# Kernel optimization log

Hardware: AMD Instinct MI355X
Metric: run time of the kernel (lower is better)

Reference implementation:

```python
import jax, jax.numpy as jnp
import numpy as np

THRESH = 0.7  # similarity_threshold from __init__
EPS = 1e-8    # torch cosine_similarity eps


def setup_inputs() -> dict:
    key = jax.random.key(0)
    ks = jax.random.split(key, 7)
    B, D, F, H, M, NMEM = 65536, 512, 10, 512, 256, 1024
    return {
        "query_features": jax.random.normal(ks[0], (B, D), jnp.float32),
        "B_mat": jax.random.normal(ks[1], (D, F), jnp.float32),
        "W1": jax.random.normal(ks[2], (2 * F, H), jnp.float32) * 0.05,
        "b1": jax.random.normal(ks[3], (H,), jnp.float32) * 0.01,
        "W2": jax.random.normal(ks[4], (H, M), jnp.float32) * 0.05,
        "b2": jax.random.normal(ks[5], (M,), jnp.float32) * 0.01,
        "memory_bank": jax.random.normal(ks[6], (NMEM, M), jnp.float32),
    }


def reference(query_features, B_mat, W1, b1, W2, b2, memory_bank):
    # Fourier features (eq. 8): [B, 2F]
    xp = query_features @ B_mat
    ff = jnp.concatenate([jnp.sin(xp), jnp.cos(xp)], axis=-1)
    # memory_net MLP -> query vectors [B, M]
    h = jax.nn.relu(ff @ W1 + b1)
    q = h @ W2 + b2
    # cosine similarity q vs memory bank (torch semantics: dot / max(|a||b|, eps))
    qn = jnp.linalg.norm(q, axis=-1, keepdims=True)          # [B,1]
    mn = jnp.linalg.norm(memory_bank, axis=-1, keepdims=True)  # [N,1]
    sim = (q @ memory_bank.T) / jnp.maximum(qn * mn.T, EPS)   # [B,N]
    max_sim = jnp.max(sim, axis=1)                            # [B]
    max_idx = jnp.argmax(sim, axis=1)                         # [B]
    relevant = memory_bank[max_idx]                           # [B,M] gather
    relevant = jnp.where((max_sim < THRESH)[:, None], 0.0, relevant)
    return relevant
```

## Files before the change

### kernel.cpp

```cpp
#include <hip/hip_runtime.h>
#include <hip/hip_bf16.h>


typedef __attribute__((ext_vector_type(8))) short short8;
typedef __attribute__((ext_vector_type(4))) float f32x4;

#define MFMA(a, b, c) __builtin_amdgcn_mfma_f32_16x16x32_bf16((a), (b), (c), 0, 0, 0)

static __device__ __forceinline__ short bfb(float f) {
  return (short)__builtin_bit_cast(unsigned short, __float2bfloat16(f));
}
static __device__ __forceinline__ unsigned short bf16bits(float f) {
  return __builtin_bit_cast(unsigned short, __float2bfloat16(f));
}
static __device__ __forceinline__ float sel10(const float a[10], int i) {
  float v = a[0];
#pragma unroll
  for (int j = 1; j < 10; ++j) v = (i == j) ? a[j] : v;
  return v;
}

typedef const __attribute__((address_space(1))) unsigned int* gas_p;
typedef __attribute__((address_space(3))) unsigned int* las_p;
static __device__ __forceinline__ void async16(const void* g, void* l) {
  __builtin_amdgcn_global_load_lds((gas_p)g, (las_p)l, 16, 0, 0);
}

__global__ __launch_bounds__(256) void prep_ff_kernel(
    const float* __restrict__ W1, const float* __restrict__ b1,
    const float* __restrict__ W2, const float* __restrict__ mem,
    const float* __restrict__ query, const float* __restrict__ Bmat,
    __hip_bfloat16* __restrict__ W1p, __hip_bfloat16* __restrict__ W2p,
    __hip_bfloat16* __restrict__ Mp, __hip_bfloat16* __restrict__ ff) {
  __shared__ __align__(16) float Bl[10 * 512];
  const int b = blockIdx.x, tid = threadIdx.x;
  if (b < 16) {
    float* invl = Bl;
    const int w = tid >> 6, lane = tid & 63, g = lane >> 4, jj = lane & 15;
    {
      int r = w * 16 + jj;
      const float4* m4 = (const float4*)(mem + (size_t)(b * 64 + r) * 256);
      float ss = 0.f;
      for (int t = 0; t < 16; ++t) {
        float4 v = m4[g * 16 + t];
        ss += v.x * v.x + v.y * v.y + v.z * v.z + v.w * v.w;
      }
      ss += __shfl_xor(ss, 16);
      ss += __shfl_xor(ss, 32);
      if (g == 0) invl[r] = rsqrtf(fmaxf(ss, 1e-30f));
    }
    __syncthreads();
    for (int u = 0; u < 64; ++u) {
      int t = u * 256 + tid;
      int j = t & 7, lane2 = (t >> 3) & 63, kt = (t >> 9) & 7, nl = t >> 12;
      int g2 = lane2 >> 4, jp = lane2 & 15;
      int nloc = nl * 16 + jp;
      int kap = 32 * kt + 16 * (j >> 2) + 4 * g2 + (j & 3);
      float v = mem[(size_t)(b * 64 + nloc) * 256 + kap] * invl[nloc];
      Mp[(size_t)b * 16384 + t] = __float2bfloat16(v);
    }
  } else if (b == 16) {
    for (int idx = tid; idx < 16384; idx += 256) {
      int j = idx & 7, lane2 = (idx >> 3) & 63, ct = idx >> 9;
      int g2 = lane2 >> 4, jp = lane2 & 15;
      int k = 8 * g2 + j;
      float v = 0.f;
      if (k < 20) v = W1[k * 512 + ct * 16 + jp];
      else if (k == 20) v = b1[ct * 16 + jp];
      W1p[idx] = __float2bfloat16(v);
    }
  } else if (b < 33) {
    int bb = b - 17;
    for (int u = 0; u < 32; ++u) {
      int idx = bb * 8192 + u * 256 + tid;
      int j = idx & 7, lane2 = (idx >> 3) & 63, c = (idx >> 9) & 15, kt = idx >> 13;
      int g2 = lane2 >> 4, jp = lane2 & 15;
      int kap = 32 * kt + 16 * (j >> 2) + 4 * g2 + (j & 3);
      W2p[idx] = __float2bfloat16(W2[(size_t)kap * 256 + c * 16 + jp]);
    }
  } else {
    const int bb = b - 33;
    for (int i = tid; i < 5120; i += 256) {
      int d = i / 10, f = i - d * 10;
      Bl[f * 512 + d] = Bmat[i];
    }
    __syncthreads();
    const int wv = tid >> 6, lane = tid & 63;
    const int g = lane >> 4, jj = lane & 15;
    const long r0 = (long)bb * 32 + (wv * 4 + g) * 2;
    const float4* qa = (const float4*)(query + r0 * 512);
    const float4* qb = (const float4*)(query + (r0 + 1) * 512);

    float acc[2][10];
#pragma unroll
    for (int f = 0; f < 10; ++f) { acc[0][f] = 0.f; acc[1][f] = 0.f; }
#pragma unroll
    for (int k = 0; k < 8; ++k) {
      float4 va = qa[jj + 16 * k];
      float4 vb = qb[jj + 16 * k];
#pragma unroll
      for (int f = 0; f < 10; ++f) {
        float4 bv = *(const float4*)(Bl + f * 512 + 4 * (jj + 16 * k));
        acc[0][f] = fmaf(va.x, bv.x, fmaf(va.y, bv.y, fmaf(va.z, bv.z, fmaf(va.w, bv.w, acc[0][f]))));
        acc[1][f] = fmaf(vb.x, bv.x, fmaf(vb.y, bv.y, fmaf(vb.z, bv.z, fmaf(vb.w, bv.w, acc[1][f]))));
      }
    }
#pragma unroll
    for (int r = 0; r < 2; ++r) {
#pragma unroll
      for (int f = 0; f < 10; ++f) {
        float s = acc[r][f];
        s += __shfl_xor(s, 1); s += __shfl_xor(s, 2);
        s += __shfl_xor(s, 4); s += __shfl_xor(s, 8);
        acc[r][f] = s;
      }
      int base = (jj < 5) ? 2 * jj : 2 * jj - 10;
      float a0 = sel10(acc[r], base);
      float a1 = sel10(acc[r], base + 1);
      float v0 = 0.f, v1 = 0.f;
      if (jj < 5) { v0 = sinf(a0); v1 = sinf(a1); }
      else if (jj < 10) { v0 = cosf(a0); v1 = cosf(a1); }
      else if (jj == 10) { v0 = 1.0f; }
      ushort2 pk;
      pk.x = bf16bits(v0);
      pk.y = bf16bits(v1);
      ((ushort2*)ff)[(r0 + r) * 16 + jj] = pk;
    }
  }
}

#define WAITV(N) asm volatile("s_waitcnt vmcnt(" #N ")" ::: "memory")
#define BAR()                        \
  do {                               \
    __builtin_amdgcn_s_barrier();    \
    asm volatile("" ::: "memory");   \
  } while (0)

#define STAGE_SLAB(s, bi)                                                       \
  do {                                                                          \
    const char* sp_ = ((s) < 32) ? (const char*)W2p + (size_t)(s) * 8192        \
                                 : (const char*)Mp + ((size_t)(s) - 32) * 8192; \
    char* dp_ = lds + 33792 + (bi) * 8192;                                      \
    async16(sp_ + tid * 16, dp_ + tid * 16);                                    \
    async16(sp_ + 4096 + tid * 16, dp_ + 4096 + tid * 16);                      \
  } while (0)

#define G3_EVEN(t, bi)                                                          \
  do {                                                                          \
    const char* buf = lds + 33792 + (bi) * 8192;                                \
    short8 a0 = *(const short8*)(lds + (size_t)(t) * 1024 + lane * 16);         \
    short8 a1 = *(const short8*)(lds + (size_t)((t) + 1) * 1024 + lane * 16);   \
    f32x4 d00 = MFMA(a0, ffq0, z4);                                             \
    f32x4 d01 = MFMA(a1, ffq0, z4);                                             \
    f32x4 d10 = MFMA(a0, ffq1, z4);                                             \
    f32x4 d11 = MFMA(a1, ffq1, z4);                                             \
    _Pragma("unroll") for (int i = 0; i < 4; ++i) {                             \
      hf0[i] = bfb(d00[i] > 0.f ? d00[i] : 0.f);                                \
      hf0[4 + i] = bfb(d01[i] > 0.f ? d01[i] : 0.f);                            \
      hf1[i] = bfb(d10[i] > 0.f ? d10[i] : 0.f);                                \
      hf1[4 + i] = bfb(d11[i] > 0.f ? d11[i] : 0.f);                            \
    }                                                                           \
    _Pragma("unroll") for (int c = 0; c < 8; ++c) {                             \
      short8 bfr = *(const short8*)(buf + c * 1024 + lane * 16);                \
      acc3a[c] = MFMA(bfr, hf0, acc3a[c]);                                      \
      acc3b[c] = MFMA(bfr, hf1, acc3b[c]);                                      \
    }                                                                           \
  } while (0)

#define G3_ODD(bi)                                                              \
  do {                                                                          \
    const char* buf = lds + 33792 + (bi) * 8192;                                \
    _Pragma("unroll") for (int c = 0; c < 8; ++c) {                             \
      short8 bfr = *(const short8*)(buf + c * 1024 + lane * 16);                \
      acc3a[8 + c] = MFMA(bfr, hf0, acc3a[8 + c]);                              \
      acc3b[8 + c] = MFMA(bfr, hf1, acc3b[8 + c]);                              \
    }                                                                           \
  } while (0)

#define G4(t, bi)                                                               \
  do {                                                                          \
    const char* buf = lds + 33792 + (bi) * 8192;                                \
    f32x4 a40 = z4, a41 = z4;                                                   \
    _Pragma("unroll") for (int kt = 0; kt < 8; ++kt) {                          \
      short8 bfr = *(const short8*)(buf + kt * 1024 + lane * 16);               \
      a40 = MFMA(qfrag0[kt], bfr, a40);                                         \
      a41 = MFMA(qfrag1[kt], bfr, a41);                                         \
    }                                                                           \
    const int n_ = ((t) - 32) * 16 + jj;                                        \
    _Pragma("unroll") for (int i = 0; i < 4; ++i) {                             \
      if (a40[i] > runmax0[i]) { runmax0[i] = a40[i]; runidx0[i] = n_; }        \
      if (a41[i] > runmax1[i]) { runmax1[i] = a41[i]; runidx1[i] = n_; }        \
    }                                                                           \
  } while (0)

__global__ __launch_bounds__(256, 2) void mega_kernel(
    const __hip_bfloat16* __restrict__ ff, const __hip_bfloat16* __restrict__ W1p,
    const __hip_bfloat16* __restrict__ W2p, const float* __restrict__ b2,
    const __hip_bfloat16* __restrict__ Mp, const float* __restrict__ mem,
    float* __restrict__ out) {
  __shared__ __align__(16) char lds[66560];
  const int tid = threadIdx.x, w = tid >> 6, lane = tid & 63;
  const int g = lane >> 4, jj = lane & 15;
  const int rowBase = blockIdx.x * 128 + w * 32;
  const f32x4 z4 = {0.f, 0.f, 0.f, 0.f};

  short8 ffq0 = *(const short8*)(ff + (size_t)(rowBase + jj) * 32 + g * 8);
  short8 ffq1 = *(const short8*)(ff + (size_t)(rowBase + 16 + jj) * 32 + g * 8);
  {
    float v = b2[tid];
    *(float*)(lds + 32768 + tid * 4) = v;
  }
#pragma unroll
  for (int r = 0; r < 8; ++r)
    async16((const char*)W1p + r * 4096 + tid * 16, lds + r * 4096 + tid * 16);
  STAGE_SLAB(0, 0);
  STAGE_SLAB(1, 1);
  STAGE_SLAB(2, 2);

  f32x4 acc3a[16], acc3b[16];
#pragma unroll
  for (int c = 0; c < 16; ++c) { acc3a[c] = z4; acc3b[c] = z4; }
  short8 hf0, hf1;

  for (int it = 0; it < 8; ++it) {
    const int t0 = it * 4;
    WAITV(4); BAR(); STAGE_SLAB(t0 + 3, 3); G3_EVEN(t0, 0);
    WAITV(4); BAR(); STAGE_SLAB(t0 + 4, 0); G3_ODD(1);
    WAITV(4); BAR(); STAGE_SLAB(t0 + 5, 1); G3_EVEN(t0 + 2, 2);
    WAITV(4); BAR(); STAGE_SLAB(t0 + 6, 2); G3_ODD(3);
  }

  short8 qfrag0[8], qfrag1[8];
  float invqn0, invqn1;
  {
    const float* b2l = (const float*)(lds + 32768);
    float qn0 = 0.f, qn1 = 0.f;
#pragma unroll
    for (int c = 0; c < 16; ++c) {
      f32x4 bb = *(const f32x4*)(b2l + c * 16 + 4 * g);
#pragma unroll
      for (int i = 0; i < 4; ++i) {
        float v0 = acc3a[c][i] + bb[i];
        float v1 = acc3b[c][i] + bb[i];
        qn0 += v0 * v0;
        qn1 += v1 * v1;
        qfrag0[c >> 1][(c & 1) * 4 + i] = bfb(v0);
        qfrag1[c >> 1][(c & 1) * 4 + i] = bfb(v1);
      }
    }
    qn0 += __shfl_xor(qn0, 16); qn0 += __shfl_xor(qn0, 32);
    qn1 += __shfl_xor(qn1, 16); qn1 += __shfl_xor(qn1, 32);
    invqn0 = rsqrtf(fmaxf(qn0, 1e-30f));
    invqn1 = rsqrtf(fmaxf(qn1, 1e-30f));
  }

  float runmax0[4], runmax1[4];
  int runidx0[4], runidx1[4];
#pragma unroll
  for (int i = 0; i < 4; ++i) {
    runmax0[i] = -1e30f; runidx0[i] = 0;
    runmax1[i] = -1e30f; runidx1[i] = 0;
  }

  for (int it = 0; it < 15; ++it) {
    const int t0 = 32 + it * 4;
    WAITV(4); BAR(); STAGE_SLAB(t0 + 3, 3); G4(t0, 0);
    WAITV(4); BAR(); STAGE_SLAB(t0 + 4, 0); G4(t0 + 1, 1);
    WAITV(4); BAR(); STAGE_SLAB(t0 + 5, 1); G4(t0 + 2, 2);
    WAITV(4); BAR(); STAGE_SLAB(t0 + 6, 2); G4(t0 + 3, 3);
  }
  WAITV(4); BAR(); STAGE_SLAB(95, 3); G4(92, 0);
  WAITV(4); BAR(); G4(93, 1);
  WAITV(2); BAR(); G4(94, 2);
  WAITV(0); BAR(); G4(95, 3);

  const float4* mem4 = (const float4*)mem;
  float4* out4 = (float4*)out;
#pragma unroll
  for (int rt = 0; rt < 2; ++rt) {
    float* rmax = rt ? runmax1 : runmax0;
    int* ridx = rt ? runidx1 : runidx0;
    float iqv = rt ? invqn1 : invqn0;
#pragma unroll
    for (int i = 0; i < 4; ++i) {
#pragma unroll
      for (int o = 1; o < 16; o <<= 1) {
        float v2 = __shfl_xor(rmax[i], o);
        int i2 = __shfl_xor(ridx[i], o);
        if (v2 > rmax[i] || (v2 == rmax[i] && i2 < ridx[i])) {
          rmax[i] = v2;
          ridx[i] = i2;
        }
      }
    }
#pragma unroll
    for (int i = 0; i < 4; ++i) {
      float iq = __shfl(iqv, 4 * g + i, 64);
      float ms = rmax[i] * iq;
      int s = (ms < 0.7f) ? -1 : ridx[i];
      size_t row = (size_t)rowBase + rt * 16 + 4 * g + i;
#pragma unroll
      for (int cq = 0; cq < 4; ++cq) {
        int col = cq * 16 + jj;
        float4 v = {0.f, 0.f, 0.f, 0.f};
        if (s >= 0) v = mem4[(size_t)s * 64 + col];
        out4[row * 64 + col] = v;
      }
    }
  }
}

extern "C" void kernel_launch(void* const* d_in, const int* in_sizes, int n_in,
                              void* d_out, int out_size, void* d_ws, size_t ws_size,
                              hipStream_t stream) {
  const float* query = (const float*)d_in[0];
  const float* Bmat = (const float*)d_in[1];
  const float* W1 = (const float*)d_in[2];
  const float* b1 = (const float*)d_in[3];
  const float* W2 = (const float*)d_in[4];
  const float* b2 = (const float*)d_in[5];
  const float* mem = (const float*)d_in[6];
  float* out = (float*)d_out;

  char* ws = (char*)d_ws;
  __hip_bfloat16* ff = (__hip_bfloat16*)ws;
  __hip_bfloat16* Mp = (__hip_bfloat16*)(ws + 4194304);
  __hip_bfloat16* W2p = (__hip_bfloat16*)(ws + 4194304 + 524288);
  __hip_bfloat16* W1p = (__hip_bfloat16*)(ws + 4194304 + 786432);

  prep_ff_kernel<<<dim3(2081), dim3(256), 0, stream>>>(W1, b1, W2, mem, query,
                                                       Bmat, W1p, W2p, Mp, ff);
  mega_kernel<<<dim3(512), dim3(256), 0, stream>>>(ff, W1p, W2p, b2, Mp, mem, out);
}
```

Baseline: 95.75 us.

## Load memory-bank fragments directly into registers instead of staging through LDS

The similarity phase stops staging memory-bank slabs through shared memory with barriers. Each wave now double-buffers its B fragments in registers, reading them straight from global/L2 while the MFMAs run on the previous tile. The W2 phase gets an explicit drain tail to match. This removes LDS traffic and block-wide barriers from the longest loop. In exchange every wave reads the whole bank from cache separately, and 16 extra short8 registers per lane raise VGPR pressure under the 2-block launch bound.

```diff
diff --git a/kernel.cpp b/kernel.cpp
--- a/kernel.cpp
+++ b/kernel.cpp
@@ -136,13 +136,12 @@
     asm volatile("" ::: "memory");   \
   } while (0)
 
-#define STAGE_SLAB(s, bi)                                                       \
-  do {                                                                          \
-    const char* sp_ = ((s) < 32) ? (const char*)W2p + (size_t)(s) * 8192        \
-                                 : (const char*)Mp + ((size_t)(s) - 32) * 8192; \
-    char* dp_ = lds + 33792 + (bi) * 8192;                                      \
-    async16(sp_ + tid * 16, dp_ + tid * 16);                                    \
-    async16(sp_ + 4096 + tid * 16, dp_ + 4096 + tid * 16);                      \
+#define STAGE_SLAB(s, bi)                                          \
+  do {                                                             \
+    const char* sp_ = (const char*)W2p + (size_t)(s) * 8192;       \
+    char* dp_ = lds + 33792 + (bi) * 8192;                         \
+    async16(sp_ + tid * 16, dp_ + tid * 16);                       \
+    async16(sp_ + 4096 + tid * 16, dp_ + 4096 + tid * 16);         \
   } while (0)
 
 #define G3_EVEN(t, bi)                                                          \
@@ -177,14 +176,19 @@
     }                                                                           \
   } while (0)
 
-#define G4(t, bi)                                                               \
+#define LOADF8(dst, t)                                                          \
   do {                                                                          \
-    const char* buf = lds + 33792 + (bi) * 8192;                                \
+    _Pragma("unroll") for (int kt = 0; kt < 8; ++kt)                            \
+      dst[kt] = *(const short8*)(mpg + (size_t)((t) - 32) * 8192 +              \
+                                 kt * 1024 + lane * 16);                        \
+  } while (0)
+
+#define G4R(buf, t)                                                             \
+  do {                                                                          \
     f32x4 a40 = z4, a41 = z4;                                                   \
     _Pragma("unroll") for (int kt = 0; kt < 8; ++kt) {                          \
-      short8 bfr = *(const short8*)(buf + kt * 1024 + lane * 16);               \
-      a40 = MFMA(qfrag0[kt], bfr, a40);                                         \
-      a41 = MFMA(qfrag1[kt], bfr, a41);                                         \
+      a40 = MFMA(qfrag0[kt], buf[kt], a40);                                     \
+      a41 = MFMA(qfrag1[kt], buf[kt], a41);                                     \
     }                                                                           \
     const int n_ = ((t) - 32) * 16 + jj;                                        \
     _Pragma("unroll") for (int i = 0; i < 4; ++i) {                             \
@@ -222,13 +226,17 @@
   for (int c = 0; c < 16; ++c) { acc3a[c] = z4; acc3b[c] = z4; }
   short8 hf0, hf1;
 
-  for (int it = 0; it < 8; ++it) {
+  for (int it = 0; it < 7; ++it) {
     const int t0 = it * 4;
     WAITV(4); BAR(); STAGE_SLAB(t0 + 3, 3); G3_EVEN(t0, 0);
     WAITV(4); BAR(); STAGE_SLAB(t0 + 4, 0); G3_ODD(1);
     WAITV(4); BAR(); STAGE_SLAB(t0 + 5, 1); G3_EVEN(t0 + 2, 2);
     WAITV(4); BAR(); STAGE_SLAB(t0 + 6, 2); G3_ODD(3);
   }
+  WAITV(4); BAR(); STAGE_SLAB(31, 3); G3_EVEN(28, 0);
+  WAITV(4); BAR(); G3_ODD(1);
+  WAITV(2); BAR(); G3_EVEN(30, 2);
+  WAITV(0); BAR(); G3_ODD(3);
 
   short8 qfrag0[8], qfrag1[8];
   float invqn0, invqn1;
@@ -262,17 +270,19 @@
     runmax1[i] = -1e30f; runidx1[i] = 0;
   }
 
-  for (int it = 0; it < 15; ++it) {
-    const int t0 = 32 + it * 4;
-    WAITV(4); BAR(); STAGE_SLAB(t0 + 3, 3); G4(t0, 0);
-    WAITV(4); BAR(); STAGE_SLAB(t0 + 4, 0); G4(t0 + 1, 1);
-    WAITV(4); BAR(); STAGE_SLAB(t0 + 5, 1); G4(t0 + 2, 2);
-    WAITV(4); BAR(); STAGE_SLAB(t0 + 6, 2); G4(t0 + 3, 3);
-  }
-  WAITV(4); BAR(); STAGE_SLAB(95, 3); G4(92, 0);
-  WAITV(4); BAR(); G4(93, 1);
-  WAITV(2); BAR(); G4(94, 2);
-  WAITV(0); BAR(); G4(95, 3);
+  const char* mpg = (const char*)Mp;
+  short8 bufA[8], bufB[8];
+  LOADF8(bufA, 32);
+  for (int it = 0; it < 31; ++it) {
+    const int s = 32 + 2 * it;
+    LOADF8(bufB, s + 1);
+    G4R(bufA, s);
+    LOADF8(bufA, s + 2);
+    G4R(bufB, s + 1);
+  }
+  LOADF8(bufB, 95);
+  G4R(bufA, 94);
+  G4R(bufB, 95);
 
   const float4* mem4 = (const float4*)mem;
   float4* out4 = (float4*)out;
```

Measured after the change: 102.0 us. +6.6%, slower.
